# Kernel optimization log

Measured on AMD Instinct MI355X. Metric: run time of the kernel, lower is better.

## Reference

```python
import jax, jax.numpy as jnp
import numpy as np

B, S, NB = 2, 1024, 64
V, D, L, H, F = 1024, 512, 12, 8, 2048
DH = D // H
MAX_BARS = 256


def _ln(x, g, b):
    m = x.mean(-1, keepdims=True)
    v = ((x - m) ** 2).mean(-1, keepdims=True)
    return (x - m) * jax.lax.rsqrt(v + 1e-5) * g + b


def _rope(x, pos):
    # x: (B, T, H, DH), pos: (T,)
    half = x.shape[-1] // 2
    inv = 10000.0 ** (-jnp.arange(half, dtype=jnp.float32) / half)
    f = pos.astype(jnp.float32)[:, None] * inv  # (T, half)
    cos = jnp.cos(f)[None, :, None, :]
    sin = jnp.sin(f)[None, :, None, :]
    x1, x2 = x[..., :half], x[..., half:]
    return jnp.concatenate([x1 * cos - x2 * sin, x1 * sin + x2 * cos], -1)


def _swiglu(h, w1, w3, w2):
    return (jax.nn.silu(h @ w1) * (h @ w3)) @ w2


def _attention(sum_x, x, Wq, Wk, Wv, Wo, smask, umask, pos_s, pos_r):
    # shared QKV/O projections over both streams; 4-way block mask via concat keys
    b, nb, _ = sum_x.shape
    s = x.shape[1]

    def proj(t, W):
        return (t @ W).reshape(t.shape[0], t.shape[1], H, DH)

    qs = _rope(proj(sum_x, Wq), pos_s)
    qr = _rope(proj(x, Wq), pos_r)
    k = jnp.concatenate([_rope(proj(sum_x, Wk), pos_s), _rope(proj(x, Wk), pos_r)], 1)
    v = jnp.concatenate([proj(sum_x, Wv), proj(x, Wv)], 1)
    scale = DH ** -0.5

    def attend(q, mask):
        sc = jnp.einsum('bqhd,bkhd->bhqk', q, k) * scale
        sc = jnp.where(mask[:, None], sc, -1e9)
        p = jax.nn.softmax(sc, axis=-1)
        o = jnp.einsum('bhqk,bkhd->bqhd', p, v)
        return o.reshape(q.shape[0], q.shape[1], D)

    return attend(qs, smask) @ Wo, attend(qr, umask) @ Wo


def _forward(tok_emb, inst_emb, bar_emb,
             ln_as_g, ln_as_b, ln_ar_g, ln_ar_b,
             ln_fs_g, ln_fs_b, ln_fr_g, ln_fr_b,
             Wq, Wk, Wv, Wo,
             fs_w1, fs_w3, fs_w2, fr_w1, fr_w3, fr_w2,
             out_g, out_b,
             token_ids, chord_ids, instrument_ids, num_bars):
    b, s = token_ids.shape
    nb = num_bars
    x = tok_emb[token_ids] + inst_emb[jnp.clip(instrument_ids, 0, 129)]
    sum_x = jnp.broadcast_to(bar_emb[:nb][None], (b, nb, tok_emb.shape[1]))

    bars = jnp.arange(nb)
    idx = jnp.arange(s)
    # ss: summary b attends summaries b' <= b (causal over bars)
    ss = jnp.broadcast_to(jnp.tril(jnp.ones((nb, nb), bool))[None], (b, nb, nb))
    # sr: summary b summarizes regular tokens in bar b
    sr = chord_ids[:, None, :] == bars[None, :, None]  # (B, nb, S)
    smask = jnp.concatenate([ss, sr], -1)  # (B, nb, nb+S)
    # rs: regular i attends summaries of strictly previous bars
    rs = bars[None, None, :] < chord_ids[:, :, None]  # (B, S, nb)
    # rr: regular i attends regular j in same bar, causally
    rr = (chord_ids[:, :, None] == chord_ids[:, None, :]) & (idx[:, None] >= idx[None, :])
    umask = jnp.concatenate([rs, rr], -1)  # (B, S, nb+S)

    pos_s = jnp.arange(nb)
    pos_r = jnp.arange(s)

    for l in range(Wq.shape[0]):
        a_s, a_r = _attention(_ln(sum_x, ln_as_g[l], ln_as_b[l]),
                              _ln(x, ln_ar_g[l], ln_ar_b[l]),
                              Wq[l], Wk[l], Wv[l], Wo[l], smask, umask, pos_s, pos_r)
        sum_x = sum_x + a_s
        x = x + a_r
        sum_x = sum_x + _swiglu(_ln(sum_x, ln_fs_g[l], ln_fs_b[l]), fs_w1[l], fs_w3[l], fs_w2[l])
        x = x + _swiglu(_ln(x, ln_fr_g[l], ln_fr_b[l]), fr_w1[l], fr_w3[l], fr_w2[l])

    x = _ln(x, out_g, out_b)
    return x @ tok_emb.T  # tied lm_head


def setup_inputs():
    key = jax.random.key(0)
    it = iter(jax.random.split(key, 40))

    def nrm(shape):
        return jax.random.normal(next(it), shape, jnp.float32) * 0.02

    inp = {
        'token_ids': jax.random.randint(next(it), (B, S), 0, V),
        'chord_ids': jnp.sort(jax.random.randint(next(it), (B, S), 0, NB), axis=-1),
        'instrument_ids': jax.random.randint(next(it), (B, S), 0, 130),
        'num_bars': NB,
        'tok_emb': nrm((V, D)),
        'inst_emb': nrm((130, D)),
        'bar_emb': nrm((MAX_BARS, D)),
        'ln_as_g': jnp.ones((L, D)), 'ln_as_b': jnp.zeros((L, D)),
        'ln_ar_g': jnp.ones((L, D)), 'ln_ar_b': jnp.zeros((L, D)),
        'ln_fs_g': jnp.ones((L, D)), 'ln_fs_b': jnp.zeros((L, D)),
        'ln_fr_g': jnp.ones((L, D)), 'ln_fr_b': jnp.zeros((L, D)),
        'Wq': nrm((L, D, D)), 'Wk': nrm((L, D, D)),
        'Wv': nrm((L, D, D)), 'Wo': nrm((L, D, D)),
        'fs_w1': nrm((L, D, F)), 'fs_w3': nrm((L, D, F)), 'fs_w2': nrm((L, F, D)),
        'fr_w1': nrm((L, D, F)), 'fr_w3': nrm((L, D, F)), 'fr_w2': nrm((L, F, D)),
        'out_g': jnp.ones((D,)), 'out_b': jnp.zeros((D,)),
    }
    return inp


def reference(token_ids, chord_ids, instrument_ids, num_bars,
              tok_emb, inst_emb, bar_emb,
              ln_as_g, ln_as_b, ln_ar_g, ln_ar_b,
              ln_fs_g, ln_fs_b, ln_fr_g, ln_fr_b,
              Wq, Wk, Wv, Wo,
              fs_w1, fs_w3, fs_w2, fr_w1, fr_w3, fr_w2,
              out_g, out_b):
    return _forward(tok_emb, inst_emb, bar_emb,
                    ln_as_g, ln_as_b, ln_ar_g, ln_ar_b,
                    ln_fs_g, ln_fs_b, ln_fr_g, ln_fr_b,
                    Wq, Wk, Wv, Wo,
                    fs_w1, fs_w3, fs_w2, fr_w1, fr_w3, fr_w2,
                    out_g, out_b,
                    token_ids, chord_ids, instrument_ids, num_bars)
```

## Files before the change

### kernel.cpp

```cpp
#include <hip/hip_runtime.h>
#include <stdint.h>

#define NB 64
#define BATCH 2
#define SEQ 1024
#define DMODEL 512
#define NHEAD 8
#define DHEAD 64
#define FDIM 2048
#define NLAYER 12
#define VOCAB 1024
#define KTOT (NB + SEQ)
#define RSUM (BATCH * NB)
#define RREG (BATCH * SEQ)
#define RTOT (RSUM + RREG)

using bf16x8 = __attribute__((ext_vector_type(8))) short;
using bf16x4 = __attribute__((ext_vector_type(4))) short;
using f32x4  = __attribute__((ext_vector_type(4))) float;

__device__ __forceinline__ unsigned short f2bf(float f) {
  union { float f; unsigned u; } c; c.f = f;
  return (unsigned short)((c.u + 0x7fffu + ((c.u >> 16) & 1u)) >> 16);
}
__device__ __forceinline__ float bf2f(unsigned short s) {
  union { unsigned u; float f; } c; c.u = ((unsigned)s) << 16;
  return c.f;
}

template<int R>
__device__ __forceinline__ void stage_tile(
    const unsigned short* __restrict__ G, int K, int base_row, int k0,
    unsigned short (*lds)[64], int wid, int lane)
{
  const int rl = lane >> 3;
  const int j  = lane & 7;
  #pragma unroll
  for (int c = 0; c < R / 32; ++c) {
    const int r0 = wid * (R / 4) + c * 8;
    const int row = r0 + rl;
    const unsigned short* g = G + (size_t)(base_row + row) * K + k0
                                + ((j ^ (row & 7)) << 3);
    __builtin_amdgcn_global_load_lds(
        (const __attribute__((address_space(1))) void*)g,
        (__attribute__((address_space(3))) void*)&lds[r0][0], 16, 0, 0);
  }
}

__device__ __forceinline__ bf16x8 lds_frag(const unsigned short (*lds)[64],
                                           int row, int cc) {
  return *(const bf16x8*)&lds[row][(cc ^ (row & 7)) << 3];
}

template<int BM, int BN, int EPI, bool PIPE>
__global__ __launch_bounds__(256) void gemm_bt(
    const unsigned short* __restrict__ A, const unsigned short* __restrict__ B0,
    const unsigned short* __restrict__ B1,
    void* __restrict__ Cout, const float* resid, int N, int K,
    const float* __restrict__ cost, const float* __restrict__ sint,
    unsigned short* __restrict__ kcat, unsigned short* __restrict__ vcat)
{
  constexpr int BK = 64;
  constexpr int WM = BM / 2, WN = BN / 2;
  constexpr int FM = WM / 16, FN = WN / 16;
  constexpr int HALF = (BM + BN) * BK * 2;
  constexpr int SM_STAGE = (PIPE ? 2 : 1) * HALF;
  constexpr int SM_CT = (EPI == 3) ? 64 * 66 * 4 : 0;
  constexpr int SMSZ = SM_STAGE > SM_CT ? SM_STAGE : SM_CT;
  __shared__ __align__(16) unsigned char smem[SMSZ];
  const int bm = blockIdx.y * BM, bn = blockIdx.x * BN;
  const unsigned short* __restrict__ BT = (bm < RSUM) ? B0 : B1;
  const int tid = threadIdx.x;
  const int wid = tid >> 6, lane = tid & 63;
  const int wm = wid >> 1, wn = wid & 1;
  const int lr = lane & 15, lk = lane >> 4;
  f32x4 acc[FM][FN] = {};
  if constexpr (PIPE) {
    auto AsB = [&](int b) { return (unsigned short (*)[BK])(smem + b * HALF); };
    auto BsB = [&](int b) { return (unsigned short (*)[BK])(smem + b * HALF + BM * BK * 2); };
    stage_tile<BM>(A,  K, bm, 0, AsB(0), wid, lane);
    stage_tile<BN>(BT, K, bn, 0, BsB(0), wid, lane);
    __syncthreads();
    int cur = 0;
    for (int k0 = 0; k0 < K; k0 += BK) {
      if (k0 + BK < K) {
        stage_tile<BM>(A,  K, bm, k0 + BK, AsB(cur ^ 1), wid, lane);
        stage_tile<BN>(BT, K, bn, k0 + BK, BsB(cur ^ 1), wid, lane);
      }
      #pragma unroll
      for (int kk = 0; kk < 2; ++kk) {
        bf16x8 af[FM], bfr[FN];
        #pragma unroll
        for (int m = 0; m < FM; ++m)
          af[m] = lds_frag(AsB(cur), wm * WM + m * 16 + lr, kk * 4 + lk);
        #pragma unroll
        for (int n = 0; n < FN; ++n)
          bfr[n] = lds_frag(BsB(cur), wn * WN + n * 16 + lr, kk * 4 + lk);
        #pragma unroll
        for (int m = 0; m < FM; ++m)
          #pragma unroll
          for (int n = 0; n < FN; ++n)
            acc[m][n] = __builtin_amdgcn_mfma_f32_16x16x32_bf16(af[m], bfr[n], acc[m][n], 0, 0, 0);
      }
      __syncthreads();
      cur ^= 1;
    }
  } else {
    auto As = (unsigned short (*)[BK])smem;
    auto Bs = (unsigned short (*)[BK])(smem + BM * BK * 2);
    for (int k0 = 0; k0 < K; k0 += BK) {
      __syncthreads();
      stage_tile<BM>(A,  K, bm, k0, As, wid, lane);
      stage_tile<BN>(BT, K, bn, k0, Bs, wid, lane);
      __syncthreads();
      #pragma unroll
      for (int kk = 0; kk < 2; ++kk) {
        bf16x8 af[FM], bfr[FN];
        #pragma unroll
        for (int m = 0; m < FM; ++m)
          af[m] = lds_frag(As, wm * WM + m * 16 + lr, kk * 4 + lk);
        #pragma unroll
        for (int n = 0; n < FN; ++n)
          bfr[n] = lds_frag(Bs, wn * WN + n * 16 + lr, kk * 4 + lk);
        #pragma unroll
        for (int m = 0; m < FM; ++m)
          #pragma unroll
          for (int n = 0; n < FN; ++n)
            acc[m][n] = __builtin_amdgcn_mfma_f32_16x16x32_bf16(af[m], bfr[n], acc[m][n], 0, 0, 0);
      }
    }
  }
  if constexpr (EPI == 3) {
    __syncthreads();
    auto ct = (float (*)[66])smem;
    #pragma unroll
    for (int m = 0; m < FM; ++m)
      #pragma unroll
      for (int n = 0; n < FN; ++n)
        #pragma unroll
        for (int i = 0; i < 4; ++i)
          ct[wm * WM + m * 16 + lk * 4 + i][wn * WN + n * 16 + lr] = acc[m][n][i];
    __syncthreads();
    const int r = tid >> 2, quad = tid & 3;
    const int tr = bm + r;
    int b, pos, catrow;
    if (tr < RSUM) { b = tr >> 6; pos = tr & (NB - 1); catrow = pos; }
    else { const int rr = tr - RSUM; b = rr >> 10; pos = rr & (SEQ - 1); catrow = NB + pos; }
    const int part = bn >> 9;
    const int head = (bn & 511) >> 6;
    const size_t obase = ((size_t)(b * NHEAD + head) * KTOT + catrow) * DHEAD + quad * 16;
    union { unsigned short u[16]; uint4 q[2]; } ob;
    if (part == 2) {
      #pragma unroll
      for (int j = 0; j < 16; ++j) ob.u[j] = f2bf(ct[r][quad * 16 + j]);
      *(uint4*)&vcat[obase] = ob.q[0];
      *(uint4*)&vcat[obase + 8] = ob.q[1];
    } else {
      #pragma unroll
      for (int j = 0; j < 16; ++j) {
        const int d = quad * 16 + j;
        const float v = ct[r][d];
        const float other = ct[r][d ^ 32];
        const float cs = cost[pos * 32 + (d & 31)];
        const float sn = sint[pos * 32 + (d & 31)];
        ob.u[j] = f2bf((d < 32) ? (v * cs - other * sn) : (other * sn + v * cs));
      }
      unsigned short* dst = part ? kcat : (unsigned short*)Cout;
      *(uint4*)&dst[obase] = ob.q[0];
      *(uint4*)&dst[obase + 8] = ob.q[1];
    }
    return;
  }
  #pragma unroll
  for (int m = 0; m < FM; ++m)
    #pragma unroll
    for (int n = 0; n < FN; ++n)
      #pragma unroll
      for (int i = 0; i < 4; ++i) {
        int row = bm + wm * WM + m * 16 + lk * 4 + i;
        int col = bn + wn * WN + n * 16 + lr;
        float v = acc[m][n][i];
        if constexpr (EPI == 1) {
          const float other = __shfl_xor(v, 1, 64);
          if (!(lr & 1)) {
            const float g = v, u = other;
            const float hv = (g / (1.f + __expf(-g))) * u;
            unsigned short* C = (unsigned short*)Cout;
            C[(size_t)row * (N >> 1) + (col >> 1)] = f2bf(hv);
          }
        } else if constexpr (EPI == 2) {
          unsigned short* C = (unsigned short*)Cout;
          C[(size_t)row * N + col] = f2bf(v);
        } else {
          float* C = (float*)Cout;
          size_t idx = (size_t)row * N + col;
          if (resid) v += resid[idx];
          C[idx] = v;
        }
      }
}

__global__ __launch_bounds__(256) void transpose_conv4_kernel(
    const float* __restrict__ s0, const float* __restrict__ s1,
    const float* __restrict__ s2, const float* __restrict__ s3,
    unsigned short* d0, unsigned short* d1,
    unsigned short* d2, unsigned short* d3,
    int K, int N, size_t sstride,
    size_t ds0, size_t ds1, size_t ds2, size_t ds3,
    int rmul, int4 radds, int nlayer)
{
  __shared__ float tile[64][65];
  const int fam = blockIdx.z / nlayer, l = blockIdx.z % nlayer;
  const float* s = (fam == 0 ? s0 : fam == 1 ? s1 : fam == 2 ? s2 : s3)
                   + (size_t)l * sstride;
  unsigned short* d = (fam == 0 ? d0 : fam == 1 ? d1 : fam == 2 ? d2 : d3)
                   + (size_t)l * (fam == 0 ? ds0 : fam == 1 ? ds1 : fam == 2 ? ds2 : ds3);
  const int radd = fam == 0 ? radds.x : fam == 1 ? radds.y : fam == 2 ? radds.z : radds.w;
  const int k0 = blockIdx.y * 64, n0 = blockIdx.x * 64;
  const int rr = threadIdx.x >> 4, c4 = threadIdx.x & 15;
  #pragma unroll
  for (int it = 0; it < 4; ++it) {
    const int r = rr + it * 16;
    *(float4*)&tile[r][c4 * 4] = *(const float4*)&s[(size_t)(k0 + r) * N + n0 + c4 * 4];
  }
  __syncthreads();
  const int n = threadIdx.x >> 2, j = threadIdx.x & 3;
  union { unsigned short u[16]; uint4 q[2]; } ob;
  #pragma unroll
  for (int i = 0; i < 16; ++i) ob.u[i] = f2bf(tile[j * 16 + i][n]);
  unsigned short* drow = d + ((size_t)(n0 + n) * rmul + radd) * K + k0 + j * 16;
  *(uint4*)&drow[0] = ob.q[0];
  *(uint4*)&drow[8] = ob.q[1];
}

__global__ __launch_bounds__(256) void convert_bf16_kernel(
    const float* __restrict__ src, unsigned short* __restrict__ dst)
{
  const int i = (blockIdx.x * 256 + threadIdx.x) * 4;
  const float4 v = *(const float4*)&src[i];
  union { unsigned short u[4]; uint2 q; } o;
  o.u[0] = f2bf(v.x); o.u[1] = f2bf(v.y); o.u[2] = f2bf(v.z); o.u[3] = f2bf(v.w);
  *(uint2*)&dst[i] = o.q;
}

__global__ __launch_bounds__(128) void embed_kernel(
    const int* __restrict__ tok, const int* __restrict__ inst,
    const float* __restrict__ tok_emb, const float* __restrict__ inst_emb,
    const float* __restrict__ bar_emb, float* __restrict__ z)
{
  const int r = blockIdx.x, t = threadIdx.x;
  float4 val;
  if (r < RSUM) {
    const int bar = r & (NB - 1);
    val = *(const float4*)&bar_emb[(size_t)bar * DMODEL + t * 4];
  } else {
    const int rr = r - RSUM;
    const int b = rr >> 10, i = rr & (SEQ - 1);
    const int tk = tok[b * SEQ + i];
    int ins = inst[b * SEQ + i];
    ins = ins < 0 ? 0 : (ins > 129 ? 129 : ins);
    const float4 a = *(const float4*)&tok_emb[(size_t)tk * DMODEL + t * 4];
    const float4 cc = *(const float4*)&inst_emb[(size_t)ins * DMODEL + t * 4];
    val.x = a.x + cc.x; val.y = a.y + cc.y; val.z = a.z + cc.z; val.w = a.w + cc.w;
  }
  *(float4*)&z[(size_t)r * DMODEL + t * 4] = val;
}

__global__ __launch_bounds__(256) void ln_dual_kernel(
    const float* __restrict__ x, const float* __restrict__ g_s,
    const float* __restrict__ b_s, const float* __restrict__ g_r,
    const float* __restrict__ b_r, unsigned short* __restrict__ out)
{
  const int wid = threadIdx.x >> 6, lane = threadIdx.x & 63;
  const size_t row = (size_t)blockIdx.x * 4 + wid;
  const float* g = (row < RSUM) ? g_s : g_r;
  const float* bb = (row < RSUM) ? b_s : b_r;
  const float* xr = x + row * DMODEL + lane * 8;
  float v[8];
  *(float4*)&v[0] = *(const float4*)&xr[0];
  *(float4*)&v[4] = *(const float4*)&xr[4];
  float s = 0.f;
  #pragma unroll
  for (int j = 0; j < 8; ++j) s += v[j];
  #pragma unroll
  for (int o = 32; o > 0; o >>= 1) s += __shfl_xor(s, o, 64);
  const float mean = s * (1.f / DMODEL);
  float vs = 0.f;
  #pragma unroll
  for (int j = 0; j < 8; ++j) { float d = v[j] - mean; vs += d * d; }
  #pragma unroll
  for (int o = 32; o > 0; o >>= 1) vs += __shfl_xor(vs, o, 64);
  const float rs = rsqrtf(vs * (1.f / DMODEL) + 1e-5f);
  float gg[8], bv[8];
  *(float4*)&gg[0] = *(const float4*)&g[lane * 8];
  *(float4*)&gg[4] = *(const float4*)&g[lane * 8 + 4];
  *(float4*)&bv[0] = *(const float4*)&bb[lane * 8];
  *(float4*)&bv[4] = *(const float4*)&bb[lane * 8 + 4];
  union { unsigned short u[8]; uint4 q; } o8;
  #pragma unroll
  for (int j = 0; j < 8; ++j) o8.u[j] = f2bf((v[j] - mean) * rs * gg[j] + bv[j]);
  *(uint4*)&out[row * DMODEL + lane * 8] = o8.q;
}

__global__ __launch_bounds__(256) void ln_kernel(
    const float* __restrict__ x, const float* __restrict__ g,
    const float* __restrict__ bb, unsigned short* __restrict__ out)
{
  const int wid = threadIdx.x >> 6, lane = threadIdx.x & 63;
  const size_t row = (size_t)blockIdx.x * 4 + wid;
  const float* xr = x + row * DMODEL + lane * 8;
  float v[8];
  *(float4*)&v[0] = *(const float4*)&xr[0];
  *(float4*)&v[4] = *(const float4*)&xr[4];
  float s = 0.f;
  #pragma unroll
  for (int j = 0; j < 8; ++j) s += v[j];
  #pragma unroll
  for (int o = 32; o > 0; o >>= 1) s += __shfl_xor(s, o, 64);
  const float mean = s * (1.f / DMODEL);
  float vs = 0.f;
  #pragma unroll
  for (int j = 0; j < 8; ++j) { float d = v[j] - mean; vs += d * d; }
  #pragma unroll
  for (int o = 32; o > 0; o >>= 1) vs += __shfl_xor(vs, o, 64);
  const float rs = rsqrtf(vs * (1.f / DMODEL) + 1e-5f);
  float gg[8], bv[8];
  *(float4*)&gg[0] = *(const float4*)&g[lane * 8];
  *(float4*)&gg[4] = *(const float4*)&g[lane * 8 + 4];
  *(float4*)&bv[0] = *(const float4*)&bb[lane * 8];
  *(float4*)&bv[4] = *(const float4*)&bb[lane * 8 + 4];
  union { unsigned short u[8]; uint4 q; } o8;
  #pragma unroll
  for (int j = 0; j < 8; ++j) o8.u[j] = f2bf((v[j] - mean) * rs * gg[j] + bv[j]);
  *(uint4*)&out[row * DMODEL + lane * 8] = o8.q;
}

__global__ void rope_table_kernel(float* __restrict__ cost, float* __restrict__ sint) {
  const int pos = blockIdx.x, j = threadIdx.x;
  const float inv = powf(10000.f, -(float)j / 32.f);
  const float f = (float)pos * inv;
  cost[pos * 32 + j] = cosf(f);
  sint[pos * 32 + j] = sinf(f);
}

__global__ void segstart_kernel(const int* __restrict__ chord, int* __restrict__ seg) {
  const int b = blockIdx.x, t = threadIdx.x;
  if (t <= NB) {
    int lo = 0, hi = SEQ;
    while (lo < hi) {
      int mid = (lo + hi) >> 1;
      if (chord[b * SEQ + mid] < t) lo = mid + 1; else hi = mid;
    }
    seg[b * (NB + 1) + t] = lo;
  }
}

__global__ __launch_bounds__(256) void attn_kernel(
    const unsigned short* __restrict__ q_cat, const unsigned short* __restrict__ k_cat,
    const unsigned short* __restrict__ v_cat, const int* __restrict__ seg,
    const int* __restrict__ chord, unsigned short* __restrict__ att)
{
  const int h = blockIdx.y, b = blockIdx.z;
  const int wid = threadIdx.x >> 6, lane = threadIdx.x & 63;
  const int qi = blockIdx.x * 4 + wid;
  int qrow, nsum, s0, nk, outrow;
  if (qi < NB) {
    const int c = qi;
    s0 = seg[b * (NB + 1) + c];
    const int s1 = seg[b * (NB + 1) + c + 1];
    qrow = c; nsum = c + 1; nk = nsum + (s1 - s0);
    outrow = b * NB + c;
  } else {
    const int i = qi - NB;
    const int c = chord[b * SEQ + i];
    s0 = seg[b * (NB + 1) + c];
    qrow = NB + i; nsum = c; nk = nsum + (i - s0 + 1);
    outrow = RSUM + b * SEQ + i;
  }
  const size_t bh = (size_t)(b * NHEAD + h) * KTOT * DHEAD;
  const unsigned short* __restrict__ Kp = k_cat + bh;
  const unsigned short* __restrict__ Vp = v_cat + bh;
  __shared__ __align__(16) float qsh[4][DHEAD];
  __shared__ __align__(16) float psh[4][64];
  qsh[wid][lane] = bf2f(q_cat[bh + (size_t)qrow * DHEAD + lane]) * 0.125f;
  const int lq = lane & 3;
  const int lkey = lane >> 2;
  const int kk = lane >> 4;
  const int dd = lane & 15;
  float m = -1e30f, l = 0.f;
  float4 o4 = {0.f, 0.f, 0.f, 0.f};
  for (int t0 = 0; t0 < nk; t0 += 64) {
    float sv[4];
    float tmax = -3.0e38f;
    #pragma unroll
    for (int pass = 0; pass < 4; ++pass) {
      const int t = t0 + pass * 16 + lkey;
      int kr = (t < nsum) ? t : (NB + s0 + (t - nsum));
      if (kr > KTOT - 1) kr = KTOT - 1;
      const bf16x8* krp = (const bf16x8*)(Kp + (size_t)kr * DHEAD + lq * 16);
      const bf16x8 k0v = krp[0], k1v = krp[1];
      float a = 0.f;
      #pragma unroll
      for (int d2 = 0; d2 < 8; ++d2)
        a = fmaf(qsh[wid][lq * 16 + d2], bf2f((unsigned short)k0v[d2]), a);
      #pragma unroll
      for (int d2 = 0; d2 < 8; ++d2)
        a = fmaf(qsh[wid][lq * 16 + 8 + d2], bf2f((unsigned short)k1v[d2]), a);
      a += __shfl_xor(a, 1, 64);
      a += __shfl_xor(a, 2, 64);
      sv[pass] = (t < nk) ? a : -3.0e38f;
      tmax = fmaxf(tmax, sv[pass]);
    }
    #pragma unroll
    for (int off = 32; off > 0; off >>= 1) tmax = fmaxf(tmax, __shfl_xor(tmax, off, 64));
    const float mn = fmaxf(m, tmax);
    float psum = 0.f;
    #pragma unroll
    for (int pass = 0; pass < 4; ++pass) {
      const float pp = __expf(sv[pass] - mn);
      psum += pp;
      if (lq == 0) psh[wid][pass * 16 + lkey] = pp;
    }
    psum *= 0.25f;
    #pragma unroll
    for (int off = 32; off > 0; off >>= 1) psum += __shfl_xor(psum, off, 64);
    const float scale = __expf(m - mn);
    l = l * scale + psum;
    o4.x *= scale; o4.y *= scale; o4.z *= scale; o4.w *= scale;
    m = mn;
    #pragma unroll
    for (int j = 0; j < 16; ++j) {
      const int toff = j * 4 + kk;
      const float p = psh[wid][toff];
      const int tk = t0 + toff;
      int kr = (tk < nsum) ? tk : (NB + s0 + (tk - nsum));
      if (kr > KTOT - 1) kr = KTOT - 1;
      const bf16x4 vv = *(const bf16x4*)&Vp[(size_t)kr * DHEAD + dd * 4];
      o4.x = fmaf(p, bf2f((unsigned short)vv[0]), o4.x);
      o4.y = fmaf(p, bf2f((unsigned short)vv[1]), o4.y);
      o4.z = fmaf(p, bf2f((unsigned short)vv[2]), o4.z);
      o4.w = fmaf(p, bf2f((unsigned short)vv[3]), o4.w);
    }
  }
  #pragma unroll
  for (int off = 16; off <= 32; off <<= 1) {
    o4.x += __shfl_xor(o4.x, off, 64);
    o4.y += __shfl_xor(o4.y, off, 64);
    o4.z += __shfl_xor(o4.z, off, 64);
    o4.w += __shfl_xor(o4.w, off, 64);
  }
  if (kk == 0) {
    const float invl = 1.f / l;
    union { unsigned short u[4]; uint2 q; } ob;
    ob.u[0] = f2bf(o4.x * invl); ob.u[1] = f2bf(o4.y * invl);
    ob.u[2] = f2bf(o4.z * invl); ob.u[3] = f2bf(o4.w * invl);
    *(uint2*)&att[(size_t)outrow * DMODEL + h * DHEAD + dd * 4] = ob.q;
  }
}

extern "C" void kernel_launch(void* const* d_in, const int* in_sizes, int n_in,
                              void* d_out, int out_size, void* d_ws, size_t ws_size,
                              hipStream_t stream)
{
  const int* tok      = (const int*)d_in[0];
  const int* chord    = (const int*)d_in[1];
  const int* inst     = (const int*)d_in[2];
  const float* tok_emb  = (const float*)d_in[4];
  const float* inst_emb = (const float*)d_in[5];
  const float* bar_emb  = (const float*)d_in[6];
  const float* ln_as_g = (const float*)d_in[7];
  const float* ln_as_b = (const float*)d_in[8];
  const float* ln_ar_g = (const float*)d_in[9];
  const float* ln_ar_b = (const float*)d_in[10];
  const float* ln_fs_g = (const float*)d_in[11];
  const float* ln_fs_b = (const float*)d_in[12];
  const float* ln_fr_g = (const float*)d_in[13];
  const float* ln_fr_b = (const float*)d_in[14];
  const float* Wq = (const float*)d_in[15];
  const float* Wk = (const float*)d_in[16];
  const float* Wv = (const float*)d_in[17];
  const float* Wo = (const float*)d_in[18];
  const float* fs_w1 = (const float*)d_in[19];
  const float* fs_w3 = (const float*)d_in[20];
  const float* fs_w2 = (const float*)d_in[21];
  const float* fr_w1 = (const float*)d_in[22];
  const float* fr_w3 = (const float*)d_in[23];
  const float* fr_w2 = (const float*)d_in[24];
  const float* out_g = (const float*)d_in[25];
  const float* out_b = (const float*)d_in[26];

  char* p = (char*)d_ws;
  auto alloc = [&](size_t bytes) -> void* {
    void* r = (void*)p;
    p += (bytes + 255) & ~(size_t)255;
    return r;
  };
  unsigned short* WqkvT  = (unsigned short*)alloc((size_t)NLAYER * 1536 * 512 * 2);
  unsigned short* WoT    = (unsigned short*)alloc((size_t)NLAYER * 512 * 512 * 2);
  unsigned short* fsW13T = (unsigned short*)alloc((size_t)NLAYER * 4096 * 512 * 2);
  unsigned short* frW13T = (unsigned short*)alloc((size_t)NLAYER * 4096 * 512 * 2);
  unsigned short* fsW2T  = (unsigned short*)alloc((size_t)NLAYER * 512 * 2048 * 2);
  unsigned short* frW2T  = (unsigned short*)alloc((size_t)NLAYER * 512 * 2048 * 2);
  unsigned short* tokT   = (unsigned short*)alloc((size_t)VOCAB * DMODEL * 2);
  float* z           = (float*)alloc((size_t)RTOT * DMODEL * 4);
  unsigned short* zn = (unsigned short*)alloc((size_t)RTOT * DMODEL * 2);
  unsigned short* q_cat = (unsigned short*)alloc((size_t)BATCH * NHEAD * KTOT * DHEAD * 2);
  unsigned short* k_cat = (unsigned short*)alloc((size_t)BATCH * NHEAD * KTOT * DHEAD * 2);
  unsigned short* v_cat = (unsigned short*)alloc((size_t)BATCH * NHEAD * KTOT * DHEAD * 2);
  unsigned short* att = (unsigned short*)alloc((size_t)RTOT * DMODEL * 2);
  unsigned short* h1 = (unsigned short*)alloc((size_t)RTOT * FDIM * 2);
  float* cost        = (float*)alloc((size_t)SEQ * 32 * 4);
  float* sint        = (float*)alloc((size_t)SEQ * 32 * 4);
  int* seg           = (int*)alloc((size_t)BATCH * (NB + 1) * 4);
  if ((size_t)(p - (char*)d_ws) > ws_size) return;

  transpose_conv4_kernel<<<dim3(512 / 64, 512 / 64, 4 * NLAYER), 256, 0, stream>>>(
      Wq, Wk, Wv, Wo,
      WqkvT, WqkvT + (size_t)512 * 512, WqkvT + (size_t)1024 * 512, WoT,
      512, 512, (size_t)512 * 512,
      (size_t)1536 * 512, (size_t)1536 * 512, (size_t)1536 * 512, (size_t)512 * 512,
      1, make_int4(0, 0, 0, 0), NLAYER);
  transpose_conv4_kernel<<<dim3(2048 / 64, 512 / 64, 4 * NLAYER), 256, 0, stream>>>(
      fs_w1, fs_w3, fr_w1, fr_w3,
      fsW13T, fsW13T, frW13T, frW13T,
      512, 2048, (size_t)512 * 2048,
      (size_t)4096 * 512, (size_t)4096 * 512, (size_t)4096 * 512, (size_t)4096 * 512,
      2, make_int4(0, 1, 0, 1), NLAYER);
  transpose_conv4_kernel<<<dim3(512 / 64, 2048 / 64, 2 * NLAYER), 256, 0, stream>>>(
      fs_w2, fr_w2, fs_w2, fr_w2,
      fsW2T, frW2T, fsW2T, frW2T,
      2048, 512, (size_t)2048 * 512,
      (size_t)512 * 2048, (size_t)512 * 2048, (size_t)512 * 2048, (size_t)512 * 2048,
      1, make_int4(0, 0, 0, 0), NLAYER);
  convert_bf16_kernel<<<VOCAB * DMODEL / 1024, 256, 0, stream>>>(tok_emb, tokT);

  embed_kernel<<<RTOT, 128, 0, stream>>>(tok, inst, tok_emb, inst_emb, bar_emb, z);
  rope_table_kernel<<<SEQ, 32, 0, stream>>>(cost, sint);
  segstart_kernel<<<BATCH, 128, 0, stream>>>(chord, seg);

  for (int l = 0; l < NLAYER; ++l) {
    const size_t ld = (size_t)l * DMODEL;
    ln_dual_kernel<<<RTOT / 4, 256, 0, stream>>>(z, ln_as_g + ld, ln_as_b + ld,
                                                 ln_ar_g + ld, ln_ar_b + ld, zn);
    gemm_bt<64, 64, 3, false><<<dim3(1536 / 64, RTOT / 64), 256, 0, stream>>>(
        zn, WqkvT + (size_t)l * 1536 * 512, WqkvT + (size_t)l * 1536 * 512,
        q_cat, nullptr, 1536, 512, cost, sint, k_cat, v_cat);
    attn_kernel<<<dim3(KTOT / 4, NHEAD, BATCH), 256, 0, stream>>>(q_cat, k_cat, v_cat, seg, chord, att);
    gemm_bt<32, 32, 0, true><<<dim3(512 / 32, RTOT / 32), 256, 0, stream>>>(
        att, WoT + (size_t)l * 512 * 512, WoT + (size_t)l * 512 * 512,
        z, z, 512, 512, nullptr, nullptr, nullptr, nullptr);
    ln_dual_kernel<<<RTOT / 4, 256, 0, stream>>>(z, ln_fs_g + ld, ln_fs_b + ld,
                                                 ln_fr_g + ld, ln_fr_b + ld, zn);
    gemm_bt<64, 64, 1, false><<<dim3(4096 / 64, RTOT / 64), 256, 0, stream>>>(
        zn, fsW13T + (size_t)l * 4096 * 512, frW13T + (size_t)l * 4096 * 512,
        h1, nullptr, 4096, 512, nullptr, nullptr, nullptr, nullptr);
    gemm_bt<32, 32, 0, true><<<dim3(512 / 32, RTOT / 32), 256, 0, stream>>>(
        h1, fsW2T + (size_t)l * 512 * 2048, frW2T + (size_t)l * 512 * 2048,
        z, z, 512, 2048, nullptr, nullptr, nullptr, nullptr);
  }

  ln_kernel<<<RREG / 4, 256, 0, stream>>>(z + (size_t)RSUM * DMODEL, out_g, out_b,
                                          zn + (size_t)RSUM * DMODEL);
  gemm_bt<32, 32, 0, true><<<dim3(VOCAB / 32, RREG / 32), 256, 0, stream>>>(
      zn + (size_t)RSUM * DMODEL, tokT, tokT, (float*)d_out, nullptr, VOCAB, 512,
      nullptr, nullptr, nullptr, nullptr);
}
```

Before: 1.223 ms.

## Store transposed weights in 64x64 blocked tiles for contiguous GEMM B loads

The weight transpose kernels now write bf16 weights as contiguous 64x64 tiles ordered by (k-tile, n-tile), with W1/W3 interleaved inside each tile. The GEMM gains a blocked B-staging path that reads each 64x64 tile as one contiguous 8 KB chunk, replacing strided row reads. The aim is better DRAM/L2 locality and fewer TLB/page crossings when loading weights. It adds template complexity, and the layout must match the existing SwiGLU epilogue's even/odd column pairing.

Measured after the change: 1.224 ms. Within noise of the previous version (+0.1%).

```diff
diff --git a/kernel.cpp b/kernel.cpp
--- a/kernel.cpp
+++ b/kernel.cpp
@@ -47,16 +47,37 @@
   }
 }
 
+template<int R>
+__device__ __forceinline__ void stage_tile_blk(
+    const unsigned short* __restrict__ G, int ntiles, int tile_n, int bnoff,
+    int k0, unsigned short (*lds)[64], int wid, int lane)
+{
+  const unsigned short* __restrict__ T =
+      G + ((size_t)(k0 >> 6) * ntiles + tile_n) * 4096;
+  const int rl = lane >> 3;
+  const int j  = lane & 7;
+  #pragma unroll
+  for (int c = 0; c < R / 32; ++c) {
+    const int r0 = wid * (R / 4) + c * 8;
+    const int row = r0 + rl;
+    const unsigned short* g = T + (size_t)(bnoff + row) * 64
+                                + ((j ^ (row & 7)) << 3);
+    __builtin_amdgcn_global_load_lds(
+        (const __attribute__((address_space(1))) void*)g,
+        (__attribute__((address_space(3))) void*)&lds[r0][0], 16, 0, 0);
+  }
+}
+
 __device__ __forceinline__ bf16x8 lds_frag(const unsigned short (*lds)[64],
                                            int row, int cc) {
   return *(const bf16x8*)&lds[row][(cc ^ (row & 7)) << 3];
 }
 
-template<int BM, int BN, int EPI, bool PIPE>
+template<int BM, int BN, int EPI, bool PIPE, bool BBLK>
 __global__ __launch_bounds__(256) void gemm_bt(
     const unsigned short* __restrict__ A, const unsigned short* __restrict__ B0,
     const unsigned short* __restrict__ B1,
-    void* __restrict__ Cout, const float* resid, int N, int K,
+    void* __restrict__ Cout, const float* resid, int N, int K, int nbt,
     const float* __restrict__ cost, const float* __restrict__ sint,
     unsigned short* __restrict__ kcat, unsigned short* __restrict__ vcat)
 {
@@ -70,22 +91,27 @@
   __shared__ __align__(16) unsigned char smem[SMSZ];
   const int bm = blockIdx.y * BM, bn = blockIdx.x * BN;
   const unsigned short* __restrict__ BT = (bm < RSUM) ? B0 : B1;
+  const int tn = bn >> 6, bnoff = bn & 63;
   const int tid = threadIdx.x;
   const int wid = tid >> 6, lane = tid & 63;
   const int wm = wid >> 1, wn = wid & 1;
   const int lr = lane & 15, lk = lane >> 4;
   f32x4 acc[FM][FN] = {};
+  auto stageB = [&](int k0, unsigned short (*lds)[64]) {
+    if constexpr (BBLK) stage_tile_blk<BN>(BT, nbt, tn, bnoff, k0, lds, wid, lane);
+    else stage_tile<BN>(BT, K, bn, k0, lds, wid, lane);
+  };
   if constexpr (PIPE) {
     auto AsB = [&](int b) { return (unsigned short (*)[BK])(smem + b * HALF); };
     auto BsB = [&](int b) { return (unsigned short (*)[BK])(smem + b * HALF + BM * BK * 2); };
-    stage_tile<BM>(A,  K, bm, 0, AsB(0), wid, lane);
-    stage_tile<BN>(BT, K, bn, 0, BsB(0), wid, lane);
+    stage_tile<BM>(A, K, bm, 0, AsB(0), wid, lane);
+    stageB(0, BsB(0));
     __syncthreads();
     int cur = 0;
     for (int k0 = 0; k0 < K; k0 += BK) {
       if (k0 + BK < K) {
-        stage_tile<BM>(A,  K, bm, k0 + BK, AsB(cur ^ 1), wid, lane);
-        stage_tile<BN>(BT, K, bn, k0 + BK, BsB(cur ^ 1), wid, lane);
+        stage_tile<BM>(A, K, bm, k0 + BK, AsB(cur ^ 1), wid, lane);
+        stageB(k0 + BK, BsB(cur ^ 1));
       }
       #pragma unroll
       for (int kk = 0; kk < 2; ++kk) {
@@ -110,8 +136,8 @@
     auto Bs = (unsigned short (*)[BK])(smem + BM * BK * 2);
     for (int k0 = 0; k0 < K; k0 += BK) {
       __syncthreads();
-      stage_tile<BM>(A,  K, bm, k0, As, wid, lane);
-      stage_tile<BN>(BT, K, bn, k0, Bs, wid, lane);
+      stage_tile<BM>(A, K, bm, k0, As, wid, lane);
+      stageB(k0, Bs);
       __syncthreads();
       #pragma unroll
       for (int kk = 0; kk < 2; ++kk) {
@@ -200,35 +226,51 @@
       }
 }
 
-__global__ __launch_bounds__(256) void transpose_conv4_kernel(
-    const float* __restrict__ s0, const float* __restrict__ s1,
-    const float* __restrict__ s2, const float* __restrict__ s3,
-    unsigned short* d0, unsigned short* d1,
-    unsigned short* d2, unsigned short* d3,
-    int K, int N, size_t sstride,
-    size_t ds0, size_t ds1, size_t ds2, size_t ds3,
-    int rmul, int4 radds, int nlayer)
+template<bool ILV>
+__global__ __launch_bounds__(256) void transpose_blk_kernel(
+    const float* __restrict__ a0, const float* __restrict__ b0,
+    const float* __restrict__ a1, const float* __restrict__ b1,
+    const float* __restrict__ a2, const float* __restrict__ b2,
+    const float* __restrict__ a3, const float* __restrict__ b3,
+    unsigned short* d0_, unsigned short* d1_,
+    unsigned short* d2_, unsigned short* d3_,
+    int Nsrc, size_t sstride, size_t dstride,
+    int4 ntiles, int4 otbase, int nlayer)
 {
   __shared__ float tile[64][65];
   const int fam = blockIdx.z / nlayer, l = blockIdx.z % nlayer;
-  const float* s = (fam == 0 ? s0 : fam == 1 ? s1 : fam == 2 ? s2 : s3)
-                   + (size_t)l * sstride;
-  unsigned short* d = (fam == 0 ? d0 : fam == 1 ? d1 : fam == 2 ? d2 : d3)
-                   + (size_t)l * (fam == 0 ? ds0 : fam == 1 ? ds1 : fam == 2 ? ds2 : ds3);
-  const int radd = fam == 0 ? radds.x : fam == 1 ? radds.y : fam == 2 ? radds.z : radds.w;
-  const int k0 = blockIdx.y * 64, n0 = blockIdx.x * 64;
+  const float* sa = (fam == 0 ? a0 : fam == 1 ? a1 : fam == 2 ? a2 : a3)
+                    + (size_t)l * sstride;
+  const float* sb = ILV ? ((fam == 0 ? b0 : fam == 1 ? b1 : fam == 2 ? b2 : b3)
+                    + (size_t)l * sstride) : nullptr;
+  unsigned short* d = (fam == 0 ? d0_ : fam == 1 ? d1_ : fam == 2 ? d2_ : d3_)
+                    + (size_t)l * dstride;
+  const int nt  = fam == 0 ? ntiles.x : fam == 1 ? ntiles.y : fam == 2 ? ntiles.z : ntiles.w;
+  const int otb = fam == 0 ? otbase.x : fam == 1 ? otbase.y : fam == 2 ? otbase.z : otbase.w;
+  const int kt = blockIdx.y, ot = blockIdx.x;
+  const int k0 = kt * 64;
   const int rr = threadIdx.x >> 4, c4 = threadIdx.x & 15;
   #pragma unroll
   for (int it = 0; it < 4; ++it) {
     const int r = rr + it * 16;
-    *(float4*)&tile[r][c4 * 4] = *(const float4*)&s[(size_t)(k0 + r) * N + n0 + c4 * 4];
+    const float* s;
+    int col0;
+    if constexpr (ILV) {
+      s = (c4 < 8) ? sa : sb;
+      col0 = ot * 32 + (c4 & 7) * 4;
+    } else {
+      s = sa;
+      col0 = ot * 64 + c4 * 4;
+    }
+    *(float4*)&tile[r][c4 * 4] = *(const float4*)&s[(size_t)(k0 + r) * Nsrc + col0];
   }
   __syncthreads();
-  const int n = threadIdx.x >> 2, j = threadIdx.x & 3;
+  const int r = threadIdx.x >> 2, j = threadIdx.x & 3;
+  const int col = ILV ? ((r >> 1) | ((r & 1) << 5)) : r;
   union { unsigned short u[16]; uint4 q[2]; } ob;
   #pragma unroll
-  for (int i = 0; i < 16; ++i) ob.u[i] = f2bf(tile[j * 16 + i][n]);
-  unsigned short* drow = d + ((size_t)(n0 + n) * rmul + radd) * K + k0 + j * 16;
+  for (int i = 0; i < 16; ++i) ob.u[i] = f2bf(tile[j * 16 + i][col]);
+  unsigned short* drow = d + ((size_t)kt * nt + otb + ot) * 4096 + r * 64 + j * 16;
   *(uint4*)&drow[0] = ob.q[0];
   *(uint4*)&drow[8] = ob.q[1];
 }
@@ -514,24 +556,26 @@
   int* seg           = (int*)alloc((size_t)BATCH * (NB + 1) * 4);
   if ((size_t)(p - (char*)d_ws) > ws_size) return;
 
-  transpose_conv4_kernel<<<dim3(512 / 64, 512 / 64, 4 * NLAYER), 256, 0, stream>>>(
-      Wq, Wk, Wv, Wo,
-      WqkvT, WqkvT + (size_t)512 * 512, WqkvT + (size_t)1024 * 512, WoT,
-      512, 512, (size_t)512 * 512,
-      (size_t)1536 * 512, (size_t)1536 * 512, (size_t)1536 * 512, (size_t)512 * 512,
-      1, make_int4(0, 0, 0, 0), NLAYER);
-  transpose_conv4_kernel<<<dim3(2048 / 64, 512 / 64, 4 * NLAYER), 256, 0, stream>>>(
-      fs_w1, fs_w3, fr_w1, fr_w3,
-      fsW13T, fsW13T, frW13T, frW13T,
-      512, 2048, (size_t)512 * 2048,
-      (size_t)4096 * 512, (size_t)4096 * 512, (size_t)4096 * 512, (size_t)4096 * 512,
-      2, make_int4(0, 1, 0, 1), NLAYER);
-  transpose_conv4_kernel<<<dim3(512 / 64, 2048 / 64, 2 * NLAYER), 256, 0, stream>>>(
-      fs_w2, fr_w2, fs_w2, fr_w2,
+  transpose_blk_kernel<false><<<dim3(8, 8, 3 * NLAYER), 256, 0, stream>>>(
+      Wq, nullptr, Wk, nullptr, Wv, nullptr, nullptr, nullptr,
+      WqkvT, WqkvT, WqkvT, WqkvT,
+      512, (size_t)512 * 512, (size_t)1536 * 512,
+      make_int4(24, 24, 24, 24), make_int4(0, 8, 16, 0), NLAYER);
+  transpose_blk_kernel<false><<<dim3(8, 8, NLAYER), 256, 0, stream>>>(
+      Wo, nullptr, nullptr, nullptr, nullptr, nullptr, nullptr, nullptr,
+      WoT, WoT, WoT, WoT,
+      512, (size_t)512 * 512, (size_t)512 * 512,
+      make_int4(8, 8, 8, 8), make_int4(0, 0, 0, 0), NLAYER);
+  transpose_blk_kernel<true><<<dim3(64, 8, 2 * NLAYER), 256, 0, stream>>>(
+      fs_w1, fs_w3, fr_w1, fr_w3, nullptr, nullptr, nullptr, nullptr,
+      fsW13T, frW13T, fsW13T, frW13T,
+      2048, (size_t)512 * 2048, (size_t)4096 * 512,
+      make_int4(64, 64, 64, 64), make_int4(0, 0, 0, 0), NLAYER);
+  transpose_blk_kernel<false><<<dim3(8, 32, 2 * NLAYER), 256, 0, stream>>>(
+      fs_w2, nullptr, fr_w2, nullptr, nullptr, nullptr, nullptr, nullptr,
       fsW2T, frW2T, fsW2T, frW2T,
-      2048, 512, (size_t)2048 * 512,
-      (size_t)512 * 2048, (size_t)512 * 2048, (size_t)512 * 2048, (size_t)512 * 2048,
-      1, make_int4(0, 0, 0, 0), NLAYER);
+      512, (size_t)2048 * 512, (size_t)512 * 2048,
+      make_int4(8, 8, 8, 8), make_int4(0, 0, 0, 0), NLAYER);
   convert_bf16_kernel<<<VOCAB * DMODEL / 1024, 256, 0, stream>>>(tok_emb, tokT);
 
   embed_kernel<<<RTOT, 128, 0, stream>>>(tok, inst, tok_emb, inst_emb, bar_emb, z);
@@ -542,26 +586,26 @@
     const size_t ld = (size_t)l * DMODEL;
     ln_dual_kernel<<<RTOT / 4, 256, 0, stream>>>(z, ln_as_g + ld, ln_as_b + ld,
                                                  ln_ar_g + ld, ln_ar_b + ld, zn);
-    gemm_bt<64, 64, 3, false><<<dim3(1536 / 64, RTOT / 64), 256, 0, stream>>>(
+    gemm_bt<64, 64, 3, false, true><<<dim3(1536 / 64, RTOT / 64), 256, 0, stream>>>(
         zn, WqkvT + (size_t)l * 1536 * 512, WqkvT + (size_t)l * 1536 * 512,
-        q_cat, nullptr, 1536, 512, cost, sint, k_cat, v_cat);
+        q_cat, nullptr, 1536, 512, 24, cost, sint, k_cat, v_cat);
     attn_kernel<<<dim3(KTOT / 4, NHEAD, BATCH), 256, 0, stream>>>(q_cat, k_cat, v_cat, seg, chord, att);
-    gemm_bt<32, 32, 0, true><<<dim3(512 / 32, RTOT / 32), 256, 0, stream>>>(
+    gemm_bt<32, 32, 0, true, true><<<dim3(512 / 32, RTOT / 32), 256, 0, stream>>>(
         att, WoT + (size_t)l * 512 * 512, WoT + (size_t)l * 512 * 512,
-        z, z, 512, 512, nullptr, nullptr, nullptr, nullptr);
+        z, z, 512, 512, 8, nullptr, nullptr, nullptr, nullptr);
     ln_dual_kernel<<<RTOT / 4, 256, 0, stream>>>(z, ln_fs_g + ld, ln_fs_b + ld,
                                                  ln_fr_g + ld, ln_fr_b + ld, zn);
-    gemm_bt<64, 64, 1, false><<<dim3(4096 / 64, RTOT / 64), 256, 0, stream>>>(
+    gemm_bt<64, 64, 1, false, true><<<dim3(4096 / 64, RTOT / 64), 256, 0, stream>>>(
         zn, fsW13T + (size_t)l * 4096 * 512, frW13T + (size_t)l * 4096 * 512,
-        h1, nullptr, 4096, 512, nullptr, nullptr, nullptr, nullptr);
-    gemm_bt<32, 32, 0, true><<<dim3(512 / 32, RTOT / 32), 256, 0, stream>>>(
+        h1, nullptr, 4096, 512, 64, nullptr, nullptr, nullptr, nullptr);
+    gemm_bt<32, 32, 0, true, true><<<dim3(512 / 32, RTOT / 32), 256, 0, stream>>>(
         h1, fsW2T + (size_t)l * 512 * 2048, frW2T + (size_t)l * 512 * 2048,
-        z, z, 512, 2048, nullptr, nullptr, nullptr, nullptr);
+        z, z, 512, 2048, 8, nullptr, nullptr, nullptr, nullptr);
   }
 
   ln_kernel<<<RREG / 4, 256, 0, stream>>>(z + (size_t)RSUM * DMODEL, out_g, out_b,
                                           zn + (size_t)RSUM * DMODEL);
-  gemm_bt<32, 32, 0, true><<<dim3(VOCAB / 32, RREG / 32), 256, 0, stream>>>(
+  gemm_bt<32, 32, 0, true, false><<<dim3(VOCAB / 32, RREG / 32), 256, 0, stream>>>(
       zn + (size_t)RSUM * DMODEL, tokT, tokT, (float*)d_out, nullptr, VOCAB, 512,
-      nullptr, nullptr, nullptr, nullptr);
-}
+      0, nullptr, nullptr, nullptr, nullptr);
+}
```

## Switch QKV layout to token-major and process four heads per wave in attention

Applied to the files above, without the earlier changes.

The QKV epilogue now writes q/k/v as [batch, token, head, dhead] instead of head-major, and the attention kernel is reorganised so each wave handles one query across four heads, 16 keys per head per pass. Each lane computes a full 64-dim dot product itself, which removes the cross-lane score reductions, and the key-row indices are cached in shared memory for the V accumulation loop. The V loop is now a variable-length loop over the actual key count rather than a fixed 16-step unrolled loop. In exchange, each lane does more serial FMAs and strided K loads, and the grid has fewer, larger blocks.

Result: slower. 1.395 ms (+14.1%).

```diff
diff --git a/kernel.cpp b/kernel.cpp
--- a/kernel.cpp
+++ b/kernel.cpp
@@ -78,13 +78,13 @@
   if constexpr (PIPE) {
     auto AsB = [&](int b) { return (unsigned short (*)[BK])(smem + b * HALF); };
     auto BsB = [&](int b) { return (unsigned short (*)[BK])(smem + b * HALF + BM * BK * 2); };
-    stage_tile<BM>(A,  K, bm, 0, AsB(0), wid, lane);
+    stage_tile<BM>(A, K, bm, 0, AsB(0), wid, lane);
     stage_tile<BN>(BT, K, bn, 0, BsB(0), wid, lane);
     __syncthreads();
     int cur = 0;
     for (int k0 = 0; k0 < K; k0 += BK) {
       if (k0 + BK < K) {
-        stage_tile<BM>(A,  K, bm, k0 + BK, AsB(cur ^ 1), wid, lane);
+        stage_tile<BM>(A, K, bm, k0 + BK, AsB(cur ^ 1), wid, lane);
         stage_tile<BN>(BT, K, bn, k0 + BK, BsB(cur ^ 1), wid, lane);
       }
       #pragma unroll
@@ -110,7 +110,7 @@
     auto Bs = (unsigned short (*)[BK])(smem + BM * BK * 2);
     for (int k0 = 0; k0 < K; k0 += BK) {
       __syncthreads();
-      stage_tile<BM>(A,  K, bm, k0, As, wid, lane);
+      stage_tile<BM>(A, K, bm, k0, As, wid, lane);
       stage_tile<BN>(BT, K, bn, k0, Bs, wid, lane);
       __syncthreads();
       #pragma unroll
@@ -148,7 +148,7 @@
     else { const int rr = tr - RSUM; b = rr >> 10; pos = rr & (SEQ - 1); catrow = NB + pos; }
     const int part = bn >> 9;
     const int head = (bn & 511) >> 6;
-    const size_t obase = ((size_t)(b * NHEAD + head) * KTOT + catrow) * DHEAD + quad * 16;
+    const size_t obase = (((size_t)(b * KTOT + catrow)) * NHEAD + head) * DHEAD + quad * 16;
     union { unsigned short u[16]; uint4 q[2]; } ob;
     if (part == 2) {
       #pragma unroll
@@ -360,9 +360,10 @@
     const unsigned short* __restrict__ v_cat, const int* __restrict__ seg,
     const int* __restrict__ chord, unsigned short* __restrict__ att)
 {
-  const int h = blockIdx.y, b = blockIdx.z;
+  const int b = blockIdx.y;
   const int wid = threadIdx.x >> 6, lane = threadIdx.x & 63;
-  const int qi = blockIdx.x * 4 + wid;
+  const int qi = blockIdx.x * 2 + (wid & 1);
+  const int hb = (wid >> 1) * 4;
   int qrow, nsum, s0, nk, outrow;
   if (qi < NB) {
     const int c = qi;
@@ -377,16 +378,21 @@
     qrow = NB + i; nsum = c; nk = nsum + (i - s0 + 1);
     outrow = RSUM + b * SEQ + i;
   }
-  const size_t bh = (size_t)(b * NHEAD + h) * KTOT * DHEAD;
-  const unsigned short* __restrict__ Kp = k_cat + bh;
-  const unsigned short* __restrict__ Vp = v_cat + bh;
-  __shared__ __align__(16) float qsh[4][DHEAD];
-  __shared__ __align__(16) float psh[4][64];
-  qsh[wid][lane] = bf2f(q_cat[bh + (size_t)qrow * DHEAD + lane]) * 0.125f;
-  const int lq = lane & 3;
-  const int lkey = lane >> 2;
-  const int kk = lane >> 4;
-  const int dd = lane & 15;
+  const size_t bbase = (size_t)b * KTOT * DMODEL;
+  const unsigned short* __restrict__ Kp = k_cat + bbase;
+  const unsigned short* __restrict__ Vp = v_cat + bbase;
+  __shared__ __align__(16) float qsh[4][256];
+  __shared__ __align__(16) float psh[4][64][4];
+  __shared__ int krsh[4][64];
+  {
+    const bf16x4 qv = *(const bf16x4*)&q_cat[bbase + (size_t)qrow * DMODEL
+                                             + hb * DHEAD + lane * 4];
+    #pragma unroll
+    for (int j = 0; j < 4; ++j)
+      qsh[wid][lane * 4 + j] = bf2f((unsigned short)qv[j]) * 0.125f;
+  }
+  const int h   = lane >> 4;
+  const int k16 = lane & 15;
   float m = -1e30f, l = 0.f;
   float4 o4 = {0.f, 0.f, 0.f, 0.f};
   for (int t0 = 0; t0 < nk; t0 += 64) {
@@ -394,68 +400,60 @@
     float tmax = -3.0e38f;
     #pragma unroll
     for (int pass = 0; pass < 4; ++pass) {
-      const int t = t0 + pass * 16 + lkey;
+      const int t = t0 + pass * 16 + k16;
       int kr = (t < nsum) ? t : (NB + s0 + (t - nsum));
       if (kr > KTOT - 1) kr = KTOT - 1;
-      const bf16x8* krp = (const bf16x8*)(Kp + (size_t)kr * DHEAD + lq * 16);
-      const bf16x8 k0v = krp[0], k1v = krp[1];
+      if (h == 0) krsh[wid][pass * 16 + k16] = kr;
+      const unsigned short* kp = Kp + (size_t)kr * DMODEL + (hb + h) * DHEAD;
       float a = 0.f;
       #pragma unroll
-      for (int d2 = 0; d2 < 8; ++d2)
-        a = fmaf(qsh[wid][lq * 16 + d2], bf2f((unsigned short)k0v[d2]), a);
-      #pragma unroll
-      for (int d2 = 0; d2 < 8; ++d2)
-        a = fmaf(qsh[wid][lq * 16 + 8 + d2], bf2f((unsigned short)k1v[d2]), a);
-      a += __shfl_xor(a, 1, 64);
-      a += __shfl_xor(a, 2, 64);
+      for (int c = 0; c < 8; ++c) {
+        const bf16x8 kv = *(const bf16x8*)&kp[c * 8];
+        #pragma unroll
+        for (int j = 0; j < 8; ++j)
+          a = fmaf(qsh[wid][h * 64 + c * 8 + j], bf2f((unsigned short)kv[j]), a);
+      }
       sv[pass] = (t < nk) ? a : -3.0e38f;
       tmax = fmaxf(tmax, sv[pass]);
     }
-    #pragma unroll
-    for (int off = 32; off > 0; off >>= 1) tmax = fmaxf(tmax, __shfl_xor(tmax, off, 64));
+    tmax = fmaxf(tmax, __shfl_xor(tmax, 1, 64));
+    tmax = fmaxf(tmax, __shfl_xor(tmax, 2, 64));
+    tmax = fmaxf(tmax, __shfl_xor(tmax, 4, 64));
+    tmax = fmaxf(tmax, __shfl_xor(tmax, 8, 64));
     const float mn = fmaxf(m, tmax);
     float psum = 0.f;
     #pragma unroll
     for (int pass = 0; pass < 4; ++pass) {
       const float pp = __expf(sv[pass] - mn);
       psum += pp;
-      if (lq == 0) psh[wid][pass * 16 + lkey] = pp;
-    }
-    psum *= 0.25f;
-    #pragma unroll
-    for (int off = 32; off > 0; off >>= 1) psum += __shfl_xor(psum, off, 64);
+      psh[wid][pass * 16 + k16][h] = pp;
+    }
+    psum += __shfl_xor(psum, 1, 64);
+    psum += __shfl_xor(psum, 2, 64);
+    psum += __shfl_xor(psum, 4, 64);
+    psum += __shfl_xor(psum, 8, 64);
     const float scale = __expf(m - mn);
     l = l * scale + psum;
     o4.x *= scale; o4.y *= scale; o4.z *= scale; o4.w *= scale;
     m = mn;
-    #pragma unroll
-    for (int j = 0; j < 16; ++j) {
-      const int toff = j * 4 + kk;
-      const float p = psh[wid][toff];
-      const int tk = t0 + toff;
-      int kr = (tk < nsum) ? tk : (NB + s0 + (tk - nsum));
-      if (kr > KTOT - 1) kr = KTOT - 1;
-      const bf16x4 vv = *(const bf16x4*)&Vp[(size_t)kr * DHEAD + dd * 4];
+    const int rem = nk - t0;
+    const int kn = rem < 64 ? rem : 64;
+    for (int k = 0; k < kn; ++k) {
+      const float p = psh[wid][k][h];
+      const int kr = krsh[wid][k];
+      const bf16x4 vv = *(const bf16x4*)&Vp[(size_t)kr * DMODEL
+                                            + (hb + h) * DHEAD + k16 * 4];
       o4.x = fmaf(p, bf2f((unsigned short)vv[0]), o4.x);
       o4.y = fmaf(p, bf2f((unsigned short)vv[1]), o4.y);
       o4.z = fmaf(p, bf2f((unsigned short)vv[2]), o4.z);
       o4.w = fmaf(p, bf2f((unsigned short)vv[3]), o4.w);
     }
   }
-  #pragma unroll
-  for (int off = 16; off <= 32; off <<= 1) {
-    o4.x += __shfl_xor(o4.x, off, 64);
-    o4.y += __shfl_xor(o4.y, off, 64);
-    o4.z += __shfl_xor(o4.z, off, 64);
-    o4.w += __shfl_xor(o4.w, off, 64);
-  }
-  if (kk == 0) {
-    const float invl = 1.f / l;
-    union { unsigned short u[4]; uint2 q; } ob;
-    ob.u[0] = f2bf(o4.x * invl); ob.u[1] = f2bf(o4.y * invl);
-    ob.u[2] = f2bf(o4.z * invl); ob.u[3] = f2bf(o4.w * invl);
-    *(uint2*)&att[(size_t)outrow * DMODEL + h * DHEAD + dd * 4] = ob.q;
-  }
+  const float invl = 1.f / l;
+  union { unsigned short u[4]; uint2 q; } ob;
+  ob.u[0] = f2bf(o4.x * invl); ob.u[1] = f2bf(o4.y * invl);
+  ob.u[2] = f2bf(o4.z * invl); ob.u[3] = f2bf(o4.w * invl);
+  *(uint2*)&att[(size_t)outrow * DMODEL + (hb + h) * DHEAD + k16 * 4] = ob.q;
 }
 
 extern "C" void kernel_launch(void* const* d_in, const int* in_sizes, int n_in,
@@ -504,9 +502,9 @@
   unsigned short* tokT   = (unsigned short*)alloc((size_t)VOCAB * DMODEL * 2);
   float* z           = (float*)alloc((size_t)RTOT * DMODEL * 4);
   unsigned short* zn = (unsigned short*)alloc((size_t)RTOT * DMODEL * 2);
-  unsigned short* q_cat = (unsigned short*)alloc((size_t)BATCH * NHEAD * KTOT * DHEAD * 2);
-  unsigned short* k_cat = (unsigned short*)alloc((size_t)BATCH * NHEAD * KTOT * DHEAD * 2);
-  unsigned short* v_cat = (unsigned short*)alloc((size_t)BATCH * NHEAD * KTOT * DHEAD * 2);
+  unsigned short* q_cat = (unsigned short*)alloc((size_t)BATCH * KTOT * DMODEL * 2);
+  unsigned short* k_cat = (unsigned short*)alloc((size_t)BATCH * KTOT * DMODEL * 2);
+  unsigned short* v_cat = (unsigned short*)alloc((size_t)BATCH * KTOT * DMODEL * 2);
   unsigned short* att = (unsigned short*)alloc((size_t)RTOT * DMODEL * 2);
   unsigned short* h1 = (unsigned short*)alloc((size_t)RTOT * FDIM * 2);
   float* cost        = (float*)alloc((size_t)SEQ * 32 * 4);
@@ -545,7 +543,7 @@
     gemm_bt<64, 64, 3, false><<<dim3(1536 / 64, RTOT / 64), 256, 0, stream>>>(
         zn, WqkvT + (size_t)l * 1536 * 512, WqkvT + (size_t)l * 1536 * 512,
         q_cat, nullptr, 1536, 512, cost, sint, k_cat, v_cat);
-    attn_kernel<<<dim3(KTOT / 4, NHEAD, BATCH), 256, 0, stream>>>(q_cat, k_cat, v_cat, seg, chord, att);
+    attn_kernel<<<dim3(KTOT / 2, BATCH), 256, 0, stream>>>(q_cat, k_cat, v_cat, seg, chord, att);
     gemm_bt<32, 32, 0, true><<<dim3(512 / 32, RTOT / 32), 256, 0, stream>>>(
         att, WoT + (size_t)l * 512 * 512, WoT + (size_t)l * 512 * 512,
         z, z, 512, 512, nullptr, nullptr, nullptr, nullptr);
```
